# Optimization experiments

Measured on AMD Instinct MI355X. Metric: run time of the kernel, lower is better.

The kernel has to match this reference:

```python
import jax, jax.numpy as jnp
import numpy as np

C, HG, WG = 8, 16, 16

def grid_sample_2d(grid, coords):
    """grid: [C,HG,WG] params; coords: [B,H,W,2] in [-1,1] (x=width, y=height).
    Bilinear, align_corners=False, zero padding. Returns [B,H,W,C]."""
    g = jnp.transpose(grid, (1, 2, 0))  # [HG,WG,C]
    ix = ((coords[..., 0] + 1.0) * WG - 1.0) * 0.5
    iy = ((coords[..., 1] + 1.0) * HG - 1.0) * 0.5
    x0f = jnp.floor(ix); y0f = jnp.floor(iy)
    x0 = x0f.astype(jnp.int32); y0 = y0f.astype(jnp.int32)
    x1 = x0 + 1; y1 = y0 + 1
    wx1 = ix - x0f; wx0 = 1.0 - wx1
    wy1 = iy - y0f; wy0 = 1.0 - wy1

    def corner(yi, xi, w):
        valid = (yi >= 0) & (yi < HG) & (xi >= 0) & (xi < WG)
        yc = jnp.clip(yi, 0, HG - 1); xc = jnp.clip(xi, 0, WG - 1)
        v = g[yc, xc]  # [B,H,W,C]
        return v * (w * valid.astype(w.dtype))[..., None]

    return (corner(y0, x0, wy0 * wx0) + corner(y0, x1, wy0 * wx1) +
            corner(y1, x0, wy1 * wx0) + corner(y1, x1, wy1 * wx1))

def setup_inputs() -> dict:
    key = jax.random.key(0)
    ks = jax.random.split(key, 8)
    B, H, W = 8, 1024, 1024
    x = jax.random.uniform(ks[0], (B, H, W, 2), jnp.float32) * 2.0 - 1.0
    grid = jax.random.normal(ks[1], (C, HG, WG), jnp.float32) * 0.1
    W1 = jax.random.normal(ks[2], (16, 8), jnp.float32) * (1.0 / np.sqrt(8))
    b1 = jax.random.normal(ks[3], (16,), jnp.float32) * 0.01
    W2 = jax.random.normal(ks[4], (16, 16), jnp.float32) * (1.0 / np.sqrt(16))
    b2 = jax.random.normal(ks[5], (16,), jnp.float32) * 0.01
    W3 = jax.random.normal(ks[6], (3, 16), jnp.float32) * (1.0 / np.sqrt(16))
    b3 = jax.random.normal(ks[7], (3,), jnp.float32) * 0.01
    return {"x": x, "grid": grid, "W1": W1, "b1": b1, "W2": W2, "b2": b2, "W3": W3, "b3": b3}

def reference(x, grid, W1, b1, W2, b2, W3, b3):
    feat = grid_sample_2d(grid, x)  # [B,H,W,8]
    h = jax.nn.leaky_relu(jnp.einsum('bhwc,oc->bhwo', feat, W1) + b1, 0.2)
    h = jax.nn.leaky_relu(jnp.einsum('bhwc,oc->bhwo', h, W2) + b2, 0.2)
    y = jax.nn.sigmoid(jnp.einsum('bhwc,oc->bhwo', h, W3) + b3)  # [B,H,W,3]
    return y
```

## Files before the change

### kernel.cpp

```cpp
#include <hip/hip_runtime.h>
#include <hip/hip_fp16.h>
#include <math.h>

typedef _Float16 half8_t  __attribute__((ext_vector_type(8)));
typedef _Float16 h2_t     __attribute__((ext_vector_type(2)));
typedef float    f32x16_t __attribute__((ext_vector_type(16)));

#define NCELL 324
#define CST   24
#define G1H   (NCELL * CST)

static __device__ __forceinline__ float sigmoid_f(float z) {
    return __builtin_amdgcn_rcpf(1.0f + __expf(-z));
}
static __device__ __forceinline__ h2_t bc_h2(int v) { return __builtin_bit_cast(h2_t, v); }
static __device__ __forceinline__ int  bc_i(h2_t v) { return __builtin_bit_cast(int, v); }

static __device__ __forceinline__ h2_t pk_max(h2_t a, h2_t b) {
#if __has_builtin(__builtin_elementwise_max)
    return __builtin_elementwise_max(a, b);
#else
    h2_t r; r[0] = a[0] > b[0] ? a[0] : b[0]; r[1] = a[1] > b[1] ? a[1] : b[1]; return r;
#endif
}
static __device__ __forceinline__ h2_t mkh2(float a, float b) {
    h2_t t; t[0] = (_Float16)a; t[1] = (_Float16)b; return t;
}
static __device__ __forceinline__ float dot2f(h2_t w, h2_t h, float c) {
#if __has_builtin(__builtin_amdgcn_fdot2)
    return __builtin_amdgcn_fdot2(w, h, c, false);
#else
    return fmaf((float)w[1], (float)h[1], fmaf((float)w[0], (float)h[0], c));
#endif
}

static __device__ __forceinline__ half8_t sample_half(const _Float16* __restrict__ sG,
                                                      float2 cc, int hi) {
    float ix = fmaf(cc.x, 8.f, 8.5f);
    float iy = fmaf(cc.y, 8.f, 8.5f);
    float xf = floorf(ix), yf = floorf(iy);
    float wx1 = ix - xf, wy1 = iy - yf;
    float wx0 = 1.f - wx1, wy0 = 1.f - wy1;
    int cx = (int)xf, cy = (int)yf;
    float w00 = wy0 * wx0, w01 = wy0 * wx1, w10 = wy1 * wx0, w11 = wy1 * wx1;
    const h2_t W00 = { (_Float16)w00, (_Float16)w00 };
    const h2_t W01 = { (_Float16)w01, (_Float16)w01 };
    const h2_t W10 = { (_Float16)w10, (_Float16)w10 };
    const h2_t W11 = { (_Float16)w11, (_Float16)w11 };
    const h2_t K02 = { (_Float16)0.2f, (_Float16)0.2f };

    const _Float16* gp = sG + (cy * 18 + cx) * CST + 8 * hi;
    const int4 A = *reinterpret_cast<const int4*>(gp);
    const int4 B = *reinterpret_cast<const int4*>(gp + CST);
    const int4 C = *reinterpret_cast<const int4*>(gp + 18 * CST);
    const int4 D = *reinterpret_cast<const int4*>(gp + 19 * CST);

    auto bl = [&](int a, int b, int c, int d) -> int {
        h2_t v = bc_h2(a) * W00;
        v = bc_h2(b) * W01 + v;
        v = bc_h2(c) * W10 + v;
        v = bc_h2(d) * W11 + v;
        return bc_i(pk_max(v, v * K02));
    };
    int4 t;
    t.x = bl(A.x, B.x, C.x, D.x);
    t.y = bl(A.y, B.y, C.y, D.y);
    t.z = bl(A.z, B.z, C.z, D.z);
    t.w = bl(A.w, B.w, C.w, D.w);
    return __builtin_bit_cast(half8_t, t);
}

__global__ __launch_bounds__(64) void fuse_grid_k(const float* __restrict__ grid,
                                                  const float* __restrict__ W1,
                                                  const float* __restrict__ b1,
                                                  __half* __restrict__ G1) {
    int cell = blockIdx.x * 64 + threadIdx.x;
    if (cell >= NCELL) return;
    int yy = (cell * 3641) >> 16;
    int xx = cell - yy * 18;
    bool border = (yy == 0) | (yy == 17) | (xx == 0) | (xx == 17);
    int base = border ? 0 : ((yy - 1) * 16 + (xx - 1));
    float g[8];
    #pragma unroll
    for (int c = 0; c < 8; ++c) g[c] = grid[c * 256 + base];
    float m = border ? 0.f : 1.f;
    __align__(16) __half tmp[24];
    #pragma unroll
    for (int o = 0; o < 16; ++o) {
        float a = 0.f;
        #pragma unroll
        for (int c = 0; c < 8; ++c) a = fmaf(W1[o * 8 + c], g[c], a);
        tmp[o] = __float2half(fmaf(a, m, b1[o]));
    }
    #pragma unroll
    for (int o = 16; o < 24; ++o) tmp[o] = __float2half(0.f);
    int4* dst = reinterpret_cast<int4*>(G1 + cell * CST);
    const int4* src = reinterpret_cast<const int4*>(tmp);
    dst[0] = src[0]; dst[1] = src[1]; dst[2] = src[2];
}

__global__ __launch_bounds__(256, 4) void mlp_main(
    const float* __restrict__ xin, const __half* __restrict__ G1,
    const float* __restrict__ W2, const float* __restrict__ b2,
    const float* __restrict__ W3, const float* __restrict__ b3,
    float* __restrict__ out, int npix, int ntiles)
{
    __shared__ __align__(16) _Float16 sG[G1H];
    const int tid = threadIdx.x;

    {
        const int4* src = reinterpret_cast<const int4*>(G1);
        int4* dst = reinterpret_cast<int4*>(sG);
        #pragma unroll
        for (int k = 0; k < 4; ++k) {
            int i = tid + k * 256;
            if (i < G1H / 8) dst[i] = src[i];
        }
    }

    const int lane = tid & 63;
    const int hi   = lane >> 5;
    const int r    = lane & 31;
    const int wv   = tid >> 6;

    half8_t A2;
    #pragma unroll
    for (int j = 0; j < 8; ++j) A2[j] = (_Float16)0.f;
    if (r < 16) {
        const float4 u0 = *reinterpret_cast<const float4*>(W2 + r * 16 + hi * 8);
        const float4 u1 = *reinterpret_cast<const float4*>(W2 + r * 16 + hi * 8 + 4);
        A2[0] = (_Float16)u0.x; A2[1] = (_Float16)u0.y; A2[2] = (_Float16)u0.z; A2[3] = (_Float16)u0.w;
        A2[4] = (_Float16)u1.x; A2[5] = (_Float16)u1.y; A2[6] = (_Float16)u1.z; A2[7] = (_Float16)u1.w;
    }

    f32x16_t b2v;
    #pragma unroll
    for (int j = 0; j < 16; ++j) b2v[j] = 0.f;
    {
        const float4 q0 = *reinterpret_cast<const float4*>(b2 + 4 * hi);
        const float4 q1 = *reinterpret_cast<const float4*>(b2 + 8 + 4 * hi);
        b2v[0] = q0.x; b2v[1] = q0.y; b2v[2] = q0.z; b2v[3] = q0.w;
        b2v[4] = q1.x; b2v[5] = q1.y; b2v[6] = q1.z; b2v[7] = q1.w;
    }

    h2_t W3L[3][4];
    #pragma unroll
    for (int o = 0; o < 3; ++o) {
        const float4 u0 = *reinterpret_cast<const float4*>(W3 + o * 16 + 4 * hi);
        const float4 u1 = *reinterpret_cast<const float4*>(W3 + o * 16 + 8 + 4 * hi);
        W3L[o][0] = mkh2(u0.x, u0.y); W3L[o][1] = mkh2(u0.z, u0.w);
        W3L[o][2] = mkh2(u1.x, u1.y); W3L[o][3] = mkh2(u1.z, u1.w);
    }
    const float b3s0 = b3[0], b3s1 = b3[1], b3s2 = b3[2];

    __syncthreads();

    const h2_t K02 = { (_Float16)0.2f, (_Float16)0.2f };
    const float2* xp = reinterpret_cast<const float2*>(xin);

    for (int tile = blockIdx.x; tile < ntiles; tile += gridDim.x) {
        const int wbase = tile * 1024 + wv * 256;

        float2 cc0v[4], cc1v[4];
        #pragma unroll
        for (int u = 0; u < 4; ++u) {
            int p0 = wbase + u * 64 + r;
            int p1 = p0 + 32;
            cc0v[u] = (p0 < npix) ? xp[p0] : make_float2(0.f, 0.f);
            cc1v[u] = (p1 < npix) ? xp[p1] : make_float2(0.f, 0.f);
        }

        #pragma unroll
        for (int u = 0; u < 4; ++u) {
            const int base = wbase + u * 64;

            half8_t fA = sample_half(sG, cc0v[u], hi);
            half8_t fB = sample_half(sG, cc1v[u], hi);

            f32x16_t acc0 = __builtin_amdgcn_mfma_f32_32x32x16_f16(A2, fA, b2v, 0, 0, 0);
            f32x16_t acc1 = __builtin_amdgcn_mfma_f32_32x32x16_f16(A2, fB, b2v, 0, 0, 0);

            h2_t hA[4], hB[4];
            #pragma unroll
            for (int p = 0; p < 4; ++p) {
                h2_t vA = mkh2(acc0[2 * p], acc0[2 * p + 1]);
                h2_t vB = mkh2(acc1[2 * p], acc1[2 * p + 1]);
                hA[p] = pk_max(vA, vA * K02);
                hB[p] = pk_max(vB, vB * K02);
            }

            float pA0 = dot2f(W3L[0][3], hA[3], dot2f(W3L[0][2], hA[2],
                        dot2f(W3L[0][1], hA[1], dot2f(W3L[0][0], hA[0], 0.f))));
            float pA1 = dot2f(W3L[1][3], hA[3], dot2f(W3L[1][2], hA[2],
                        dot2f(W3L[1][1], hA[1], dot2f(W3L[1][0], hA[0], 0.f))));
            float pA2 = dot2f(W3L[2][3], hA[3], dot2f(W3L[2][2], hA[2],
                        dot2f(W3L[2][1], hA[1], dot2f(W3L[2][0], hA[0], 0.f))));
            float pB0 = dot2f(W3L[0][3], hB[3], dot2f(W3L[0][2], hB[2],
                        dot2f(W3L[0][1], hB[1], dot2f(W3L[0][0], hB[0], 0.f))));
            float pB1 = dot2f(W3L[1][3], hB[3], dot2f(W3L[1][2], hB[2],
                        dot2f(W3L[1][1], hB[1], dot2f(W3L[1][0], hB[0], 0.f))));
            float pB2 = dot2f(W3L[2][3], hB[3], dot2f(W3L[2][2], hB[2],
                        dot2f(W3L[2][1], hB[1], dot2f(W3L[2][0], hB[0], 0.f))));

            float sel0 = hi ? pA0 : pB0;
            float sel1 = hi ? pA1 : pB1;
            float sel2 = hi ? pA2 : pB2;
            float got0 = __shfl_xor(sel0, 32);
            float got1 = __shfl_xor(sel1, 32);
            float got2 = __shfl_xor(sel2, 32);
            float y0 = (hi ? pB0 : pA0) + got0 + b3s0;
            float y1 = (hi ? pB1 : pA1) + got1 + b3s1;
            float y2 = (hi ? pB2 : pA2) + got2 + b3s2;

            const int pv = base + lane;
            if (pv < npix) {
                float* po = out + pv * 3;
                po[0] = sigmoid_f(y0);
                po[1] = sigmoid_f(y1);
                po[2] = sigmoid_f(y2);
            }
        }
    }
}

extern "C" void kernel_launch(void* const* d_in, const int* in_sizes, int n_in,
                              void* d_out, int out_size, void* d_ws, size_t ws_size,
                              hipStream_t stream)
{
    const float* xin  = (const float*)d_in[0];
    const float* grid = (const float*)d_in[1];
    const float* W1   = (const float*)d_in[2];
    const float* b1   = (const float*)d_in[3];
    const float* W2   = (const float*)d_in[4];
    const float* b2   = (const float*)d_in[5];
    const float* W3   = (const float*)d_in[6];
    const float* b3   = (const float*)d_in[7];
    float* out = (float*)d_out;

    int npix = in_sizes[0] / 2;
    __half* g1 = (__half*)d_ws;

    fuse_grid_k<<<(NCELL + 63) / 64, 64, 0, stream>>>(grid, W1, b1, g1);
    int ntiles = (npix + 1023) / 1024;
    int nb = ntiles < 2048 ? ntiles : 2048;
    mlp_main<<<nb, 256, 0, stream>>>(xin, g1, W2, b2, W3, b3, out, npix, ntiles);
}
```

Baseline: 68.46 us.

## Split grid gathers between LDS and global cache; launch one block per tile

Half of the bilinear corner gathers (the second pixel group) now read the fused grid table directly from global memory through the cache instead of shared memory, spreading gather traffic across the LDS and the vector memory path. The persistent grid-stride loop is removed and one block is launched per 1024-pixel tile, which gives 8192 blocks instead of 2048. This is meant to relieve LDS bandwidth and bank-conflict pressure on the random gathers. In exchange the global gathers have higher latency, and every block still copies the whole table into LDS even though it uses it for only half the samples.

```diff
diff --git a/kernel.cpp b/kernel.cpp
--- a/kernel.cpp
+++ b/kernel.cpp
@@ -34,27 +34,19 @@
 #endif
 }
 
-static __device__ __forceinline__ half8_t sample_half(const _Float16* __restrict__ sG,
-                                                      float2 cc, int hi) {
+static __device__ __forceinline__ half8_t bilerp8(int4 A, int4 B, int4 C, int4 D,
+                                                  float2 cc) {
     float ix = fmaf(cc.x, 8.f, 8.5f);
     float iy = fmaf(cc.y, 8.f, 8.5f);
     float xf = floorf(ix), yf = floorf(iy);
     float wx1 = ix - xf, wy1 = iy - yf;
     float wx0 = 1.f - wx1, wy0 = 1.f - wy1;
-    int cx = (int)xf, cy = (int)yf;
     float w00 = wy0 * wx0, w01 = wy0 * wx1, w10 = wy1 * wx0, w11 = wy1 * wx1;
     const h2_t W00 = { (_Float16)w00, (_Float16)w00 };
     const h2_t W01 = { (_Float16)w01, (_Float16)w01 };
     const h2_t W10 = { (_Float16)w10, (_Float16)w10 };
     const h2_t W11 = { (_Float16)w11, (_Float16)w11 };
     const h2_t K02 = { (_Float16)0.2f, (_Float16)0.2f };
-
-    const _Float16* gp = sG + (cy * 18 + cx) * CST + 8 * hi;
-    const int4 A = *reinterpret_cast<const int4*>(gp);
-    const int4 B = *reinterpret_cast<const int4*>(gp + CST);
-    const int4 C = *reinterpret_cast<const int4*>(gp + 18 * CST);
-    const int4 D = *reinterpret_cast<const int4*>(gp + 19 * CST);
-
     auto bl = [&](int a, int b, int c, int d) -> int {
         h2_t v = bc_h2(a) * W00;
         v = bc_h2(b) * W01 + v;
@@ -70,6 +62,33 @@
     return __builtin_bit_cast(half8_t, t);
 }
 
+static __device__ __forceinline__ int cell_of(float2 cc) {
+    float ix = fmaf(cc.x, 8.f, 8.5f);
+    float iy = fmaf(cc.y, 8.f, 8.5f);
+    int cx = (int)floorf(ix), cy = (int)floorf(iy);
+    return cy * 18 + cx;
+}
+
+static __device__ __forceinline__ half8_t sample_half_lds(const _Float16* __restrict__ sG,
+                                                          float2 cc, int hi) {
+    const _Float16* gp = sG + cell_of(cc) * CST + 8 * hi;
+    const int4 A = *reinterpret_cast<const int4*>(gp);
+    const int4 B = *reinterpret_cast<const int4*>(gp + CST);
+    const int4 C = *reinterpret_cast<const int4*>(gp + 18 * CST);
+    const int4 D = *reinterpret_cast<const int4*>(gp + 19 * CST);
+    return bilerp8(A, B, C, D, cc);
+}
+
+static __device__ __forceinline__ half8_t sample_half_g(const __half* __restrict__ G1g,
+                                                        float2 cc, int hi) {
+    const __half* gp = G1g + cell_of(cc) * CST + 8 * hi;
+    const int4 A = *reinterpret_cast<const int4*>(gp);
+    const int4 B = *reinterpret_cast<const int4*>(gp + CST);
+    const int4 C = *reinterpret_cast<const int4*>(gp + 18 * CST);
+    const int4 D = *reinterpret_cast<const int4*>(gp + 19 * CST);
+    return bilerp8(A, B, C, D, cc);
+}
+
 __global__ __launch_bounds__(64) void fuse_grid_k(const float* __restrict__ grid,
                                                   const float* __restrict__ W1,
                                                   const float* __restrict__ b1,
@@ -103,7 +122,7 @@
     const float* __restrict__ xin, const __half* __restrict__ G1,
     const float* __restrict__ W2, const float* __restrict__ b2,
     const float* __restrict__ W3, const float* __restrict__ b3,
-    float* __restrict__ out, int npix, int ntiles)
+    float* __restrict__ out, int npix)
 {
     __shared__ __align__(16) _Float16 sG[G1H];
     const int tid = threadIdx.x;
@@ -158,67 +177,64 @@
     const h2_t K02 = { (_Float16)0.2f, (_Float16)0.2f };
     const float2* xp = reinterpret_cast<const float2*>(xin);
 
-    for (int tile = blockIdx.x; tile < ntiles; tile += gridDim.x) {
-        const int wbase = tile * 1024 + wv * 256;
-
-        float2 cc0v[4], cc1v[4];
+    const int wbase = blockIdx.x * 1024 + wv * 256;
+    float2 cc0v[4], cc1v[4];
+    #pragma unroll
+    for (int u = 0; u < 4; ++u) {
+        int p0 = wbase + u * 64 + r;
+        int p1 = p0 + 32;
+        cc0v[u] = (p0 < npix) ? xp[p0] : make_float2(0.f, 0.f);
+        cc1v[u] = (p1 < npix) ? xp[p1] : make_float2(0.f, 0.f);
+    }
+
+    #pragma unroll
+    for (int u = 0; u < 4; ++u) {
+        const int base = wbase + u * 64;
+
+        half8_t fA = sample_half_lds(sG, cc0v[u], hi);
+        half8_t fB = sample_half_g(G1, cc1v[u], hi);
+
+        f32x16_t acc0 = __builtin_amdgcn_mfma_f32_32x32x16_f16(A2, fA, b2v, 0, 0, 0);
+        f32x16_t acc1 = __builtin_amdgcn_mfma_f32_32x32x16_f16(A2, fB, b2v, 0, 0, 0);
+
+        h2_t hA[4], hB[4];
         #pragma unroll
-        for (int u = 0; u < 4; ++u) {
-            int p0 = wbase + u * 64 + r;
-            int p1 = p0 + 32;
-            cc0v[u] = (p0 < npix) ? xp[p0] : make_float2(0.f, 0.f);
-            cc1v[u] = (p1 < npix) ? xp[p1] : make_float2(0.f, 0.f);
+        for (int p = 0; p < 4; ++p) {
+            h2_t vA = mkh2(acc0[2 * p], acc0[2 * p + 1]);
+            h2_t vB = mkh2(acc1[2 * p], acc1[2 * p + 1]);
+            hA[p] = pk_max(vA, vA * K02);
+            hB[p] = pk_max(vB, vB * K02);
         }
 
-        #pragma unroll
-        for (int u = 0; u < 4; ++u) {
-            const int base = wbase + u * 64;
-
-            half8_t fA = sample_half(sG, cc0v[u], hi);
-            half8_t fB = sample_half(sG, cc1v[u], hi);
-
-            f32x16_t acc0 = __builtin_amdgcn_mfma_f32_32x32x16_f16(A2, fA, b2v, 0, 0, 0);
-            f32x16_t acc1 = __builtin_amdgcn_mfma_f32_32x32x16_f16(A2, fB, b2v, 0, 0, 0);
-
-            h2_t hA[4], hB[4];
-            #pragma unroll
-            for (int p = 0; p < 4; ++p) {
-                h2_t vA = mkh2(acc0[2 * p], acc0[2 * p + 1]);
-                h2_t vB = mkh2(acc1[2 * p], acc1[2 * p + 1]);
-                hA[p] = pk_max(vA, vA * K02);
-                hB[p] = pk_max(vB, vB * K02);
-            }
-
-            float pA0 = dot2f(W3L[0][3], hA[3], dot2f(W3L[0][2], hA[2],
-                        dot2f(W3L[0][1], hA[1], dot2f(W3L[0][0], hA[0], 0.f))));
-            float pA1 = dot2f(W3L[1][3], hA[3], dot2f(W3L[1][2], hA[2],
-                        dot2f(W3L[1][1], hA[1], dot2f(W3L[1][0], hA[0], 0.f))));
-            float pA2 = dot2f(W3L[2][3], hA[3], dot2f(W3L[2][2], hA[2],
-                        dot2f(W3L[2][1], hA[1], dot2f(W3L[2][0], hA[0], 0.f))));
-            float pB0 = dot2f(W3L[0][3], hB[3], dot2f(W3L[0][2], hB[2],
-                        dot2f(W3L[0][1], hB[1], dot2f(W3L[0][0], hB[0], 0.f))));
-            float pB1 = dot2f(W3L[1][3], hB[3], dot2f(W3L[1][2], hB[2],
-                        dot2f(W3L[1][1], hB[1], dot2f(W3L[1][0], hB[0], 0.f))));
-            float pB2 = dot2f(W3L[2][3], hB[3], dot2f(W3L[2][2], hB[2],
-                        dot2f(W3L[2][1], hB[1], dot2f(W3L[2][0], hB[0], 0.f))));
-
-            float sel0 = hi ? pA0 : pB0;
-            float sel1 = hi ? pA1 : pB1;
-            float sel2 = hi ? pA2 : pB2;
-            float got0 = __shfl_xor(sel0, 32);
-            float got1 = __shfl_xor(sel1, 32);
-            float got2 = __shfl_xor(sel2, 32);
-            float y0 = (hi ? pB0 : pA0) + got0 + b3s0;
-            float y1 = (hi ? pB1 : pA1) + got1 + b3s1;
-            float y2 = (hi ? pB2 : pA2) + got2 + b3s2;
-
-            const int pv = base + lane;
-            if (pv < npix) {
-                float* po = out + pv * 3;
-                po[0] = sigmoid_f(y0);
-                po[1] = sigmoid_f(y1);
-                po[2] = sigmoid_f(y2);
-            }
+        float pA0 = dot2f(W3L[0][3], hA[3], dot2f(W3L[0][2], hA[2],
+                    dot2f(W3L[0][1], hA[1], dot2f(W3L[0][0], hA[0], 0.f))));
+        float pA1 = dot2f(W3L[1][3], hA[3], dot2f(W3L[1][2], hA[2],
+                    dot2f(W3L[1][1], hA[1], dot2f(W3L[1][0], hA[0], 0.f))));
+        float pA2 = dot2f(W3L[2][3], hA[3], dot2f(W3L[2][2], hA[2],
+                    dot2f(W3L[2][1], hA[1], dot2f(W3L[2][0], hA[0], 0.f))));
+        float pB0 = dot2f(W3L[0][3], hB[3], dot2f(W3L[0][2], hB[2],
+                    dot2f(W3L[0][1], hB[1], dot2f(W3L[0][0], hB[0], 0.f))));
+        float pB1 = dot2f(W3L[1][3], hB[3], dot2f(W3L[1][2], hB[2],
+                    dot2f(W3L[1][1], hB[1], dot2f(W3L[1][0], hB[0], 0.f))));
+        float pB2 = dot2f(W3L[2][3], hB[3], dot2f(W3L[2][2], hB[2],
+                    dot2f(W3L[2][1], hB[1], dot2f(W3L[2][0], hB[0], 0.f))));
+
+        float sel0 = hi ? pA0 : pB0;
+        float sel1 = hi ? pA1 : pB1;
+        float sel2 = hi ? pA2 : pB2;
+        float got0 = __shfl_xor(sel0, 32);
+        float got1 = __shfl_xor(sel1, 32);
+        float got2 = __shfl_xor(sel2, 32);
+        float y0 = (hi ? pB0 : pA0) + got0 + b3s0;
+        float y1 = (hi ? pB1 : pA1) + got1 + b3s1;
+        float y2 = (hi ? pB2 : pA2) + got2 + b3s2;
+
+        const int pv = base + lane;
+        if (pv < npix) {
+            float* po = out + pv * 3;
+            po[0] = sigmoid_f(y0);
+            po[1] = sigmoid_f(y1);
+            po[2] = sigmoid_f(y2);
         }
     }
 }
@@ -241,7 +257,6 @@
     __half* g1 = (__half*)d_ws;
 
     fuse_grid_k<<<(NCELL + 63) / 64, 64, 0, stream>>>(grid, W1, b1, g1);
-    int ntiles = (npix + 1023) / 1024;
-    int nb = ntiles < 2048 ? ntiles : 2048;
-    mlp_main<<<nb, 256, 0, stream>>>(xin, g1, W2, b2, W3, b3, out, npix, ntiles);
-}
+    int nb = (npix + 1023) / 1024;
+    mlp_main<<<nb, 256, 0, stream>>>(xin, g1, W2, b2, W3, b3, out, npix);
+}
```

Result: slower. 83.26 us (+21.6%).
